# Kernel tuning notes

Measured on AMD Instinct MI355X. Metric: run time of the kernel, lower is better.

Reference implementation:

```python
import jax, jax.numpy as jnp
import numpy as np

EPS = 1e-5

def conv_act_norm(x, W, b, a, g, be):
    """1x1 Conv2d -> PReLU -> LayerNormalization4D (normalize over channel dim).
    x: [B,C,T,F]; W: [O,C]; b,g,be: [O]; a: PReLU scalar."""
    y = jnp.einsum('bctf,oc->botf', x, W) + b[None, :, None, None]
    y = jnp.where(y >= 0, y, a * y)
    mu = y.mean(axis=1, keepdims=True)
    var = y.var(axis=1, keepdims=True)
    y = (y - mu) * jax.lax.rsqrt(var + EPS)
    return y * g[None, :, None, None] + be[None, :, None, None]


def setup_inputs() -> dict:
    key = jax.random.key(0)
    B, C, T, F = 2, 64, 2048, 64
    H, HC = 4, 4            # n_head, hid_chan
    VC = C // H             # value channels per head = 16
    ks = jax.random.split(key, 16)
    s = 0.05
    inp = {
        'x': jax.random.normal(ks[0], (B, C, T, F), jnp.float32),
        # per-head Q projections (stacked along leading head axis)
        'Wq': jax.random.normal(ks[1], (H, HC, C), jnp.float32) * s,
        'bq': jnp.zeros((H, HC), jnp.float32),
        'aq': jnp.full((H,), 0.25, jnp.float32),
        'gq': jnp.ones((H, HC), jnp.float32),
        'betaq': jnp.zeros((H, HC), jnp.float32),
        # per-head K projections
        'Wk': jax.random.normal(ks[2], (H, HC, C), jnp.float32) * s,
        'bk': jnp.zeros((H, HC), jnp.float32),
        'ak': jnp.full((H,), 0.25, jnp.float32),
        'gk': jnp.ones((H, HC), jnp.float32),
        'betak': jnp.zeros((H, HC), jnp.float32),
        # per-head V projections
        'Wv': jax.random.normal(ks[3], (H, VC, C), jnp.float32) * s,
        'bv': jnp.zeros((H, VC), jnp.float32),
        'av': jnp.full((H,), 0.25, jnp.float32),
        'gv': jnp.ones((H, VC), jnp.float32),
        'betav': jnp.zeros((H, VC), jnp.float32),
        # output concat projection
        'Wp': jax.random.normal(ks[4], (C, C), jnp.float32) * s,
        'bp': jnp.zeros((C,), jnp.float32),
        'ap': jnp.asarray(0.25, jnp.float32),
        'gp': jnp.ones((C,), jnp.float32),
        'betap': jnp.zeros((C,), jnp.float32),
    }
    return inp


def reference(x, Wq, bq, aq, gq, betaq, Wk, bk, ak, gk, betak,
              Wv, bv, av, gv, betav, Wp, bp, ap, gp, betap):
    H = Wq.shape[0]
    B, C, T, F = x.shape
    per_head = jax.vmap(conv_act_norm, in_axes=(None, 0, 0, 0, 0, 0))
    Q = per_head(x, Wq, bq, aq, gq, betaq)      # [H,B,HC,T,F]
    K = per_head(x, Wk, bk, ak, gk, betak)      # [H,B,HC,T,F]
    V = per_head(x, Wv, bv, av, gv, betav)      # [H,B,VC,T,F]
    # flatten: sequence over time, embedding = channels*freq
    Qf = Q.transpose(0, 1, 3, 2, 4).reshape(H, B, T, -1)   # [H,B,T,HC*F]
    Kf = K.transpose(0, 1, 3, 2, 4).reshape(H, B, T, -1)
    Vt = V.transpose(0, 1, 3, 2, 4)                          # [H,B,T,VC,F]
    Vf = Vt.reshape(H, B, T, -1)                             # [H,B,T,VC*F]
    d = Qf.shape[-1]
    scale = jnp.asarray(1.0 / np.sqrt(d), x.dtype)
    attn = jnp.einsum('hbtd,hbsd->hbts', Qf, Kf) * scale    # [H,B,T,T]
    attn = jax.nn.softmax(attn, axis=-1)
    O = jnp.einsum('hbts,hbsd->hbtd', attn, Vf).reshape(Vt.shape)  # [H,B,T,VC,F]
    # back to [B, H*VC, T, F] with head-major channel ordering (matches torch view)
    O = O.transpose(1, 0, 3, 2, 4).reshape(B, C, T, F)
    out = conv_act_norm(O, Wp, bp, ap, gp, betap)
    return out + x
```

## Files before the change

kernel.cpp:

```cpp
#include <hip/hip_runtime.h>
#include <stdint.h>

typedef unsigned short ushort_t;
typedef unsigned int u32;
typedef short bf16x8 __attribute__((ext_vector_type(8)));
typedef float f32x4 __attribute__((ext_vector_type(4)));

#define MFMA16(a, b, c) __builtin_amdgcn_mfma_f32_16x16x32_bf16((a), (b), (c), 0, 0, 0)

__device__ __forceinline__ ushort_t f2bf(float f) {
  union { float f; u32 u; } v; v.f = f;
  return (ushort_t)((v.u + 0x7FFFu + ((v.u >> 16) & 1u)) >> 16);
}
__device__ __forceinline__ float bf2f(ushort_t h) {
  union { u32 u; float f; } v; v.u = ((u32)h) << 16;
  return v.f;
}

__device__ __forceinline__ void store_frag(ushort_t* __restrict__ arr, int hb, int t, int d, float v) {
  int lane = (t & 15) | (((d >> 3) & 3) << 4);
  size_t addr = ((((size_t)hb * 128 + (t >> 4)) * 8 + (d >> 5)) << 9) + ((size_t)lane << 3) + (d & 7);
  arr[addr] = f2bf(v);
}

__global__ __launch_bounds__(256) void k_proj_qkv(
    const float* __restrict__ x,
    const float* __restrict__ Wq, const float* __restrict__ bq, const float* __restrict__ aq,
    const float* __restrict__ gq, const float* __restrict__ beq,
    const float* __restrict__ Wk, const float* __restrict__ bk, const float* __restrict__ ak,
    const float* __restrict__ gk, const float* __restrict__ bek,
    const float* __restrict__ Wv, const float* __restrict__ bv, const float* __restrict__ av,
    const float* __restrict__ gv, const float* __restrict__ bev,
    ushort_t* __restrict__ Qp, ushort_t* __restrict__ Kp,
    ushort_t* __restrict__ Vp_hi, ushort_t* __restrict__ Vp_lo)
{
  int tid = blockIdx.x * 256 + threadIdx.x;
  int f = tid & 63;
  int t = (tid >> 6) & 2047;
  int b = tid >> 17;

  float qa[16], ka[16], va[64];
#pragma unroll
  for (int o = 0; o < 16; ++o) { qa[o] = bq[o]; ka[o] = bk[o]; }
#pragma unroll
  for (int o = 0; o < 64; ++o) va[o] = bv[o];

  const float* xp = x + ((size_t)b * 64 * 2048 + t) * 64 + f;
  for (int c = 0; c < 64; ++c) {
    float xv = xp[(size_t)c * (2048 * 64)];
#pragma unroll
    for (int o = 0; o < 16; ++o) qa[o] += Wq[o * 64 + c] * xv;
#pragma unroll
    for (int o = 0; o < 16; ++o) ka[o] += Wk[o * 64 + c] * xv;
#pragma unroll
    for (int o = 0; o < 64; ++o) va[o] += Wv[o * 64 + c] * xv;
  }

#pragma unroll
  for (int h = 0; h < 4; ++h) {
    int hb = h * 2 + b;
    {
      float aa = aq[h];
      float y[4]; float mu = 0.f;
#pragma unroll
      for (int j = 0; j < 4; ++j) { float u = qa[h * 4 + j]; u = u >= 0.f ? u : aa * u; y[j] = u; mu += u; }
      mu *= 0.25f;
      float var = 0.f;
#pragma unroll
      for (int j = 0; j < 4; ++j) { float d = y[j] - mu; var += d * d; }
      float is = rsqrtf(var * 0.25f + 1e-5f);
#pragma unroll
      for (int j = 0; j < 4; ++j) {
        float v = ((y[j] - mu) * is * gq[h * 4 + j] + beq[h * 4 + j]) * 0.0625f;
        store_frag(Qp, hb, t, j * 64 + f, v);
      }
    }
    {
      float aa = ak[h];
      float y[4]; float mu = 0.f;
#pragma unroll
      for (int j = 0; j < 4; ++j) { float u = ka[h * 4 + j]; u = u >= 0.f ? u : aa * u; y[j] = u; mu += u; }
      mu *= 0.25f;
      float var = 0.f;
#pragma unroll
      for (int j = 0; j < 4; ++j) { float d = y[j] - mu; var += d * d; }
      float is = rsqrtf(var * 0.25f + 1e-5f);
#pragma unroll
      for (int j = 0; j < 4; ++j) {
        float v = (y[j] - mu) * is * gk[h * 4 + j] + bek[h * 4 + j];
        store_frag(Kp, hb, t, j * 64 + f, v);
      }
    }
    {
      float aa = av[h];
      float y[16]; float mu = 0.f;
#pragma unroll
      for (int j = 0; j < 16; ++j) { float u = va[h * 16 + j]; u = u >= 0.f ? u : aa * u; y[j] = u; mu += u; }
      mu *= 0.0625f;
      float var = 0.f;
#pragma unroll
      for (int j = 0; j < 16; ++j) { float d = y[j] - mu; var += d * d; }
      float is = rsqrtf(var * 0.0625f + 1e-5f);
      int vlane = (f & 15) | (((t >> 3) & 3) << 4);
#pragma unroll
      for (int vc = 0; vc < 16; ++vc) {
        float v = (y[vc] - mu) * is * gv[h * 16 + vc] + bev[h * 16 + vc];
        int dvt = vc * 4 + (f >> 4);
        size_t addr = ((((size_t)hb * 64 + (t >> 5)) * 64 + dvt) << 9) + ((size_t)vlane << 3) + (t & 7);
        ushort_t hh = f2bf(v);
        Vp_hi[addr] = hh;
        Vp_lo[addr] = f2bf(v - bf2f(hh));
      }
    }
  }
}

__global__ __launch_bounds__(512, 4) void k_attn(
    const ushort_t* __restrict__ Qp, const ushort_t* __restrict__ Kp,
    const ushort_t* __restrict__ Vp_hi, const ushort_t* __restrict__ Vp_lo,
    float* __restrict__ O)
{
  extern __shared__ char smem[];
  ushort_t* Kbuf = (ushort_t*)smem;
  ushort_t* Qlds = (ushort_t*)(smem + 32768);
  ushort_t* Plds = (ushort_t*)(smem + 65536);
  float* pmax  = (float*)(smem + 69632);
  float* psum  = (float*)(smem + 70144);
  float* rsrow = (float*)(smem + 70656);
  float* lrow  = (float*)(smem + 70912);

  const int lane = threadIdx.x & 63;
  const int wid  = threadIdx.x >> 6;
  const int qblk = wid >> 1;
  const int tsh  = wid & 1;
  const int hb = blockIdx.x & 7;
  const int r2 = blockIdx.x >> 3;
  const int dvh = r2 & 1;
  const int qtile = r2 >> 1;
  const int tb4 = (lane >> 4) << 2;
  const int rowbase = qblk * 16 + tb4;

  {
    const ushort_t* qsrc = Qp + (((size_t)(hb * 128 + qtile * 4)) << 12) + ((size_t)lane << 3);
#pragma unroll
    for (int i = 0; i < 4; ++i) {
      int c = wid * 4 + i;
      uint4 v = *(const uint4*)(qsrc + ((size_t)c << 9));
      *(uint4*)(Qlds + ((size_t)c << 9) + ((size_t)lane << 3)) = v;
    }
    const ushort_t* ksrc = Kp + (((size_t)(hb * 128)) << 12) + ((size_t)lane << 3);
#pragma unroll
    for (int i = 0; i < 2; ++i) {
      int c = wid * 2 + i;
      uint4 v = *(const uint4*)(ksrc + ((size_t)c << 9));
      *(uint4*)(Kbuf + ((size_t)c << 9) + ((size_t)lane << 3)) = v;
    }
  }
  __syncthreads();

  f32x4 acc[16];
#pragma unroll
  for (int i = 0; i < 16; ++i) acc[i] = (f32x4){0.f, 0.f, 0.f, 0.f};
  float m_run[4], l_run[4];
#pragma unroll
  for (int r = 0; r < 4; ++r) { m_run[r] = -1e30f; l_run[r] = 0.f; }

  for (int s = 0; s < 64; ++s) {
    uint4 kst0, kst1;
    {
      int sn = (s + 1) & 63;
      const ushort_t* ksrc = Kp + (((size_t)(hb * 128 + 2 * sn)) << 12) + ((size_t)lane << 3);
      kst0 = *(const uint4*)(ksrc + ((size_t)(wid * 2 + 0) << 9));
      kst1 = *(const uint4*)(ksrc + ((size_t)(wid * 2 + 1) << 9));
    }

    const ushort_t* kb = Kbuf + (((size_t)(s & 1)) << 13);
    f32x4 sacc = (f32x4){0.f, 0.f, 0.f, 0.f};
    __builtin_amdgcn_s_setprio(1);
#pragma unroll
    for (int kk = 0; kk < 8; ++kk) {
      bf16x8 qf = *(const bf16x8*)(Qlds + (((size_t)(qblk * 8 + kk)) << 9) + ((size_t)lane << 3));
      bf16x8 kf = *(const bf16x8*)(kb + (((size_t)(tsh * 8 + kk)) << 9) + ((size_t)lane << 3));
      sacc = MFMA16(qf, kf, sacc);
    }
    __builtin_amdgcn_s_setprio(0);
    float rm[4];
#pragma unroll
    for (int r = 0; r < 4; ++r) rm[r] = sacc[r];
#pragma unroll
    for (int m = 1; m <= 8; m <<= 1) {
#pragma unroll
      for (int r = 0; r < 4; ++r) rm[r] = fmaxf(rm[r], __shfl_xor(rm[r], m));
    }
    if ((lane & 15) == 0)
      *(f32x4*)&pmax[tsh * 64 + rowbase] = (f32x4){rm[0], rm[1], rm[2], rm[3]};
    __syncthreads();

    f32x4 pm0 = *(const f32x4*)&pmax[rowbase];
    f32x4 pm1 = *(const f32x4*)&pmax[64 + rowbase];
    float rs[4], pv[4];
#pragma unroll
    for (int r = 0; r < 4; ++r) {
      float mn = fmaxf(m_run[r], fmaxf(pm0[r], pm1[r]));
      rs[r] = __expf(m_run[r] - mn);
      m_run[r] = mn;
      pv[r] = __expf(sacc[r] - mn);
    }
    float ps[4];
#pragma unroll
    for (int r = 0; r < 4; ++r) ps[r] = pv[r];
#pragma unroll
    for (int m = 1; m <= 8; m <<= 1) {
#pragma unroll
      for (int r = 0; r < 4; ++r) ps[r] += __shfl_xor(ps[r], m);
    }
    if ((lane & 15) == 0) {
      *(f32x4*)&psum[tsh * 64 + rowbase] = (f32x4){ps[0], ps[1], ps[2], ps[3]};
      if (tsh == 0)
        *(f32x4*)&rsrow[rowbase] = (f32x4){rs[0], rs[1], rs[2], rs[3]};
    }
    {
      int ts = tsh * 16 + (lane & 15);
      int cs = (ts >> 3) << 4;
      int jj = ts & 7;
#pragma unroll
      for (int r = 0; r < 4; ++r) {
        int tgt = (tb4 + r) | cs;
        Plds[(((size_t)qblk) << 9) + (tgt << 3) + jj] = f2bf(pv[r]);
      }
    }
    __syncthreads();

    {
      ushort_t* kdst = Kbuf + (((size_t)((s + 1) & 1)) << 13) + ((size_t)lane << 3);
      *(uint4*)(kdst + ((size_t)(wid * 2 + 0) << 9)) = kst0;
      *(uint4*)(kdst + ((size_t)(wid * 2 + 1) << 9)) = kst1;
    }

    {
      {
        f32x4 s0 = *(const f32x4*)&psum[rowbase];
        f32x4 s1 = *(const f32x4*)&psum[64 + rowbase];
#pragma unroll
        for (int r = 0; r < 4; ++r) l_run[r] = l_run[r] * rs[r] + s0[r] + s1[r];
      }
      const int dvt0 = dvh * 32 + wid * 4;
      const ushort_t* vh0 = Vp_hi + ((((size_t)hb * 64 + s) * 64 + dvt0) << 9) + ((size_t)lane << 3);
      const ushort_t* vl0 = Vp_lo + ((((size_t)hb * 64 + s) * 64 + dvt0) << 9) + ((size_t)lane << 3);
#pragma unroll
      for (int ip = 0; ip < 2; ++ip) {
        bf16x8 vh_a = *(const bf16x8*)(vh0 + ((size_t)(ip * 2 + 0) << 9));
        bf16x8 vl_a = *(const bf16x8*)(vl0 + ((size_t)(ip * 2 + 0) << 9));
        bf16x8 vh_b = *(const bf16x8*)(vh0 + ((size_t)(ip * 2 + 1) << 9));
        bf16x8 vl_b = *(const bf16x8*)(vl0 + ((size_t)(ip * 2 + 1) << 9));
        __builtin_amdgcn_s_setprio(1);
#pragma unroll
        for (int q = 0; q < 4; ++q) {
          bf16x8 pf = *(const bf16x8*)(Plds + (((size_t)q) << 9) + ((size_t)lane << 3));
          f32x4 rq = *(const f32x4*)&rsrow[q * 16 + tb4];
          int ia = q * 4 + ip * 2 + 0;
          int ib = q * 4 + ip * 2 + 1;
#pragma unroll
          for (int r = 0; r < 4; ++r) { acc[ia][r] *= rq[r]; acc[ib][r] *= rq[r]; }
          acc[ia] = MFMA16(pf, vh_a, acc[ia]);
          acc[ia] = MFMA16(pf, vl_a, acc[ia]);
          acc[ib] = MFMA16(pf, vh_b, acc[ib]);
          acc[ib] = MFMA16(pf, vl_b, acc[ib]);
        }
        __builtin_amdgcn_s_setprio(0);
      }
    }
    __syncthreads();
  }

  if (tsh == 0 && (lane & 15) == 0)
    *(f32x4*)&lrow[rowbase] = (f32x4){l_run[0], l_run[1], l_run[2], l_run[3]};
  __syncthreads();

  const int h = hb >> 1, b = hb & 1;
#pragma unroll
  for (int q = 0; q < 4; ++q) {
    f32x4 lq = *(const f32x4*)&lrow[q * 16 + tb4];
    f32x4 inv;
#pragma unroll
    for (int r = 0; r < 4; ++r) inv[r] = 1.0f / lq[r];
    int trow = qtile * 64 + q * 16 + tb4;
#pragma unroll
    for (int i = 0; i < 4; ++i) {
      int dv = dvh * 512 + wid * 64 + i * 16 + (lane & 15);
      float* op = O + (((size_t)b * 64 + h * 16 + (dv >> 6)) * 2048 + trow) * 64 + (dv & 63);
#pragma unroll
      for (int r = 0; r < 4; ++r) op[(size_t)r * 64] = acc[q * 4 + i][r] * inv[r];
    }
  }
}

__global__ __launch_bounds__(256) void k_outproj(
    const float* __restrict__ O, const float* __restrict__ Wp, const float* __restrict__ bp,
    const float* __restrict__ ap, const float* __restrict__ gp, const float* __restrict__ bep,
    const float* __restrict__ x, float* __restrict__ out)
{
  int tid = blockIdx.x * 256 + threadIdx.x;
  int f = tid & 63;
  int t = (tid >> 6) & 2047;
  int b = tid >> 17;

  float acc[64];
#pragma unroll
  for (int o = 0; o < 64; ++o) acc[o] = bp[o];
  const float* op_ = O + ((size_t)b * 64 * 2048 + t) * 64 + f;
  for (int c = 0; c < 64; ++c) {
    float ov = op_[(size_t)c * (2048 * 64)];
#pragma unroll
    for (int o = 0; o < 64; ++o) acc[o] += Wp[o * 64 + c] * ov;
  }
  float aa = ap[0];
  float mu = 0.f;
#pragma unroll
  for (int o = 0; o < 64; ++o) { float y = acc[o]; y = y >= 0.f ? y : aa * y; acc[o] = y; mu += y; }
  mu *= 0.015625f;
  float var = 0.f;
#pragma unroll
  for (int o = 0; o < 64; ++o) { float d = acc[o] - mu; var += d * d; }
  float is = rsqrtf(var * 0.015625f + 1e-5f);
  size_t base = ((size_t)b * 64 * 2048 + t) * 64 + f;
#pragma unroll
  for (int o = 0; o < 64; ++o) {
    size_t idx = base + (size_t)o * (2048 * 64);
    out[idx] = (acc[o] - mu) * is * gp[o] + bep[o] + x[idx];
  }
}

extern "C" void kernel_launch(void* const* d_in, const int* in_sizes, int n_in,
                              void* d_out, int out_size, void* d_ws, size_t ws_size,
                              hipStream_t stream) {
  (void)in_sizes; (void)n_in; (void)out_size; (void)ws_size;
  const float* x   = (const float*)d_in[0];
  const float* Wq  = (const float*)d_in[1];
  const float* bq  = (const float*)d_in[2];
  const float* aq  = (const float*)d_in[3];
  const float* gq  = (const float*)d_in[4];
  const float* beq = (const float*)d_in[5];
  const float* Wk  = (const float*)d_in[6];
  const float* bk  = (const float*)d_in[7];
  const float* ak  = (const float*)d_in[8];
  const float* gk  = (const float*)d_in[9];
  const float* bek = (const float*)d_in[10];
  const float* Wv  = (const float*)d_in[11];
  const float* bv  = (const float*)d_in[12];
  const float* av  = (const float*)d_in[13];
  const float* gv  = (const float*)d_in[14];
  const float* bev = (const float*)d_in[15];
  const float* Wp  = (const float*)d_in[16];
  const float* bp  = (const float*)d_in[17];
  const float* ap  = (const float*)d_in[18];
  const float* gp  = (const float*)d_in[19];
  const float* bep = (const float*)d_in[20];

  char* ws = (char*)d_ws;
  const size_t MB = 1024 * 1024;
  ushort_t* Qp    = (ushort_t*)(ws + 0 * MB);
  ushort_t* Kp    = (ushort_t*)(ws + 8 * MB);
  ushort_t* Vp_hi = (ushort_t*)(ws + 16 * MB);
  ushort_t* Vp_lo = (ushort_t*)(ws + 48 * MB);
  float*    Obuf  = (float*)(ws + 80 * MB);

  hipFuncSetAttribute((const void*)k_attn, hipFuncAttributeMaxDynamicSharedMemorySize, 71168);

  k_proj_qkv<<<1024, 256, 0, stream>>>(x, Wq, bq, aq, gq, beq, Wk, bk, ak, gk, bek,
                                       Wv, bv, av, gv, bev, Qp, Kp, Vp_hi, Vp_lo);
  k_attn<<<512, 512, 71168, stream>>>(Qp, Kp, Vp_hi, Vp_lo, Obuf);
  k_outproj<<<1024, 256, 0, stream>>>(Obuf, Wp, bp, ap, gp, bep, x, (float*)d_out);
}
```

Before: 555.6 us.

## Drop V lo-split, store O in bf16, stage QKV via LDS, lazy softmax rescale

V is no longer split into bf16 hi/lo halves, which halves the V MFMAs and V traffic in attention. The attention output is written as bf16 instead of fp32, shrinking the intermediate buffer that outproj reads. The QKV projection kernel now loads x into registers once, loops over heads, and stages results in LDS so global stores are coalesced 16-byte writes. The online softmax skips the accumulator rescale when the running max grows by at most 8, which avoids exp and multiply work but lets exponentials grow larger. The cost is lower precision in V and O.

```diff
diff --git a/kernel.cpp b/kernel.cpp
--- a/kernel.cpp
+++ b/kernel.cpp
@@ -17,13 +17,7 @@
   return v.f;
 }
 
-__device__ __forceinline__ void store_frag(ushort_t* __restrict__ arr, int hb, int t, int d, float v) {
-  int lane = (t & 15) | (((d >> 3) & 3) << 4);
-  size_t addr = ((((size_t)hb * 128 + (t >> 4)) * 8 + (d >> 5)) << 9) + ((size_t)lane << 3) + (d & 7);
-  arr[addr] = f2bf(v);
-}
-
-__global__ __launch_bounds__(256) void k_proj_qkv(
+__global__ __launch_bounds__(512, 4) void k_proj_qkv(
     const float* __restrict__ x,
     const float* __restrict__ Wq, const float* __restrict__ bq, const float* __restrict__ aq,
     const float* __restrict__ gq, const float* __restrict__ beq,
@@ -31,94 +25,122 @@
     const float* __restrict__ gk, const float* __restrict__ bek,
     const float* __restrict__ Wv, const float* __restrict__ bv, const float* __restrict__ av,
     const float* __restrict__ gv, const float* __restrict__ bev,
-    ushort_t* __restrict__ Qp, ushort_t* __restrict__ Kp,
-    ushort_t* __restrict__ Vp_hi, ushort_t* __restrict__ Vp_lo)
+    ushort_t* __restrict__ Qp, ushort_t* __restrict__ Kp, ushort_t* __restrict__ Vp)
 {
-  int tid = blockIdx.x * 256 + threadIdx.x;
-  int f = tid & 63;
-  int t = (tid >> 6) & 2047;
-  int b = tid >> 17;
-
-  float qa[16], ka[16], va[64];
-#pragma unroll
-  for (int o = 0; o < 16; ++o) { qa[o] = bq[o]; ka[o] = bk[o]; }
-#pragma unroll
-  for (int o = 0; o < 64; ++o) va[o] = bv[o];
-
-  const float* xp = x + ((size_t)b * 64 * 2048 + t) * 64 + f;
-  for (int c = 0; c < 64; ++c) {
-    float xv = xp[(size_t)c * (2048 * 64)];
-#pragma unroll
-    for (int o = 0; o < 16; ++o) qa[o] += Wq[o * 64 + c] * xv;
-#pragma unroll
-    for (int o = 0; o < 16; ++o) ka[o] += Wk[o * 64 + c] * xv;
-#pragma unroll
-    for (int o = 0; o < 64; ++o) va[o] += Wv[o * 64 + c] * xv;
-  }
-
-#pragma unroll
+  __shared__ ushort_t lds_q[16 * 136];
+  __shared__ ushort_t lds_k[16 * 136];
+  __shared__ ushort_t lds_v[512 * 24];
+
+  const int tid = threadIdx.x;
+  const int fi = tid & 31, ti = tid >> 5;
+  const int lane = tid & 63, wid = tid >> 6;
+  const int bid = blockIdx.x;
+  const int tt = bid & 127;
+  const int fh = (bid >> 7) & 1;
+  const int b  = bid >> 8;
+  const int t = tt * 16 + ti;
+  const int f = fh * 32 + fi;
+
+  float xr[64];
+  {
+    const float* xp = x + ((size_t)b * 64 * 2048 + t) * 64 + f;
+#pragma unroll
+    for (int c = 0; c < 64; ++c) xr[c] = xp[(size_t)c * (2048 * 64)];
+  }
+
+#pragma unroll 1
   for (int h = 0; h < 4; ++h) {
-    int hb = h * 2 + b;
-    {
-      float aa = aq[h];
-      float y[4]; float mu = 0.f;
-#pragma unroll
-      for (int j = 0; j < 4; ++j) { float u = qa[h * 4 + j]; u = u >= 0.f ? u : aa * u; y[j] = u; mu += u; }
+    const int hb = h * 2 + b;
+    float qa[4], ka[4], va[16];
+#pragma unroll
+    for (int j = 0; j < 4; ++j) { qa[j] = bq[h * 4 + j]; ka[j] = bk[h * 4 + j]; }
+#pragma unroll
+    for (int j = 0; j < 16; ++j) va[j] = bv[h * 16 + j];
+    for (int c = 0; c < 64; ++c) {
+      float xv = xr[c];
+#pragma unroll
+      for (int j = 0; j < 4; ++j) qa[j] += Wq[(h * 4 + j) * 64 + c] * xv;
+#pragma unroll
+      for (int j = 0; j < 4; ++j) ka[j] += Wk[(h * 4 + j) * 64 + c] * xv;
+#pragma unroll
+      for (int j = 0; j < 16; ++j) va[j] += Wv[(h * 16 + j) * 64 + c] * xv;
+    }
+    {
+      float aa = aq[h], mu = 0.f;
+#pragma unroll
+      for (int j = 0; j < 4; ++j) { float u = qa[j]; u = u >= 0.f ? u : aa * u; qa[j] = u; mu += u; }
       mu *= 0.25f;
       float var = 0.f;
 #pragma unroll
-      for (int j = 0; j < 4; ++j) { float d = y[j] - mu; var += d * d; }
+      for (int j = 0; j < 4; ++j) { float d = qa[j] - mu; var += d * d; }
       float is = rsqrtf(var * 0.25f + 1e-5f);
 #pragma unroll
       for (int j = 0; j < 4; ++j) {
-        float v = ((y[j] - mu) * is * gq[h * 4 + j] + beq[h * 4 + j]) * 0.0625f;
-        store_frag(Qp, hb, t, j * 64 + f, v);
-      }
-    }
-    {
-      float aa = ak[h];
-      float y[4]; float mu = 0.f;
-#pragma unroll
-      for (int j = 0; j < 4; ++j) { float u = ka[h * 4 + j]; u = u >= 0.f ? u : aa * u; y[j] = u; mu += u; }
+        float v = ((qa[j] - mu) * is * gq[h * 4 + j] + beq[h * 4 + j]) * 0.0625f;
+        lds_q[ti * 136 + j * 32 + fi] = f2bf(v);
+      }
+    }
+    {
+      float aa = ak[h], mu = 0.f;
+#pragma unroll
+      for (int j = 0; j < 4; ++j) { float u = ka[j]; u = u >= 0.f ? u : aa * u; ka[j] = u; mu += u; }
       mu *= 0.25f;
       float var = 0.f;
 #pragma unroll
-      for (int j = 0; j < 4; ++j) { float d = y[j] - mu; var += d * d; }
+      for (int j = 0; j < 4; ++j) { float d = ka[j] - mu; var += d * d; }
       float is = rsqrtf(var * 0.25f + 1e-5f);
 #pragma unroll
       for (int j = 0; j < 4; ++j) {
-        float v = (y[j] - mu) * is * gk[h * 4 + j] + bek[h * 4 + j];
-        store_frag(Kp, hb, t, j * 64 + f, v);
-      }
-    }
-    {
-      float aa = av[h];
-      float y[16]; float mu = 0.f;
-#pragma unroll
-      for (int j = 0; j < 16; ++j) { float u = va[h * 16 + j]; u = u >= 0.f ? u : aa * u; y[j] = u; mu += u; }
+        float v = (ka[j] - mu) * is * gk[h * 4 + j] + bek[h * 4 + j];
+        lds_k[ti * 136 + j * 32 + fi] = f2bf(v);
+      }
+    }
+    {
+      float aa = av[h], mu = 0.f;
+#pragma unroll
+      for (int j = 0; j < 16; ++j) { float u = va[j]; u = u >= 0.f ? u : aa * u; va[j] = u; mu += u; }
       mu *= 0.0625f;
       float var = 0.f;
 #pragma unroll
-      for (int j = 0; j < 16; ++j) { float d = y[j] - mu; var += d * d; }
+      for (int j = 0; j < 16; ++j) { float d = va[j] - mu; var += d * d; }
       float is = rsqrtf(var * 0.0625f + 1e-5f);
-      int vlane = (f & 15) | (((t >> 3) & 3) << 4);
 #pragma unroll
       for (int vc = 0; vc < 16; ++vc) {
-        float v = (y[vc] - mu) * is * gv[h * 16 + vc] + bev[h * 16 + vc];
-        int dvt = vc * 4 + (f >> 4);
-        size_t addr = ((((size_t)hb * 64 + (t >> 5)) * 64 + dvt) << 9) + ((size_t)vlane << 3) + (t & 7);
-        ushort_t hh = f2bf(v);
-        Vp_hi[addr] = hh;
-        Vp_lo[addr] = f2bf(v - bf2f(hh));
-      }
-    }
+        float v = (va[vc] - mu) * is * gv[h * 16 + vc] + bev[h * 16 + vc];
+        lds_v[(vc * 32 + fi) * 24 + ti] = f2bf(v);
+      }
+    }
+    __syncthreads();
+
+    {
+      int j = wid & 3;
+      const ushort_t* src = (wid < 4) ? lds_q : lds_k;
+      uint4 v = *(const uint4*)&src[(lane & 15) * 136 + j * 32 + ((lane >> 4) << 3)];
+      size_t base = ((((size_t)hb * 128 + tt) * 8) + (2 * j + fh)) << 9;
+      ushort_t* dst = (wid < 4) ? Qp : Kp;
+      *(uint4*)(dst + base + ((size_t)lane << 3)) = v;
+    }
+    {
+      const int halfsel = tt & 1;
+      const bool act = (lane >> 5) == halfsel;
+#pragma unroll
+      for (int i = 0; i < 4; ++i) {
+        int gl = wid * 4 + i;
+        int vc = gl >> 1, u = gl & 1;
+        int row = vc * 32 + u * 16 + (lane & 15);
+        uint4 v = *(const uint4*)&lds_v[row * 24 + (((lane >> 4) & 1) << 3)];
+        int g = vc * 4 + fh * 2 + u;
+        size_t base = (((size_t)hb * 64 + (tt >> 1)) * 64 + g) << 9;
+        if (act) *(uint4*)(Vp + base + ((size_t)lane << 3)) = v;
+      }
+    }
+    __syncthreads();
   }
 }
 
 __global__ __launch_bounds__(512, 4) void k_attn(
     const ushort_t* __restrict__ Qp, const ushort_t* __restrict__ Kp,
-    const ushort_t* __restrict__ Vp_hi, const ushort_t* __restrict__ Vp_lo,
-    float* __restrict__ O)
+    const ushort_t* __restrict__ Vp, ushort_t* __restrict__ O)
 {
   extern __shared__ char smem[];
   ushort_t* Kbuf = (ushort_t*)smem;
@@ -128,6 +150,7 @@
   float* psum  = (float*)(smem + 70144);
   float* rsrow = (float*)(smem + 70656);
   float* lrow  = (float*)(smem + 70912);
+  int*   skipf = (int*)(smem + 71168);
 
   const int lane = threadIdx.x & 63;
   const int wid  = threadIdx.x >> 6;
@@ -145,15 +168,13 @@
 #pragma unroll
     for (int i = 0; i < 4; ++i) {
       int c = wid * 4 + i;
-      uint4 v = *(const uint4*)(qsrc + ((size_t)c << 9));
-      *(uint4*)(Qlds + ((size_t)c << 9) + ((size_t)lane << 3)) = v;
+      *(uint4*)(Qlds + ((size_t)c << 9) + ((size_t)lane << 3)) = *(const uint4*)(qsrc + ((size_t)c << 9));
     }
     const ushort_t* ksrc = Kp + (((size_t)(hb * 128)) << 12) + ((size_t)lane << 3);
 #pragma unroll
     for (int i = 0; i < 2; ++i) {
       int c = wid * 2 + i;
-      uint4 v = *(const uint4*)(ksrc + ((size_t)c << 9));
-      *(uint4*)(Kbuf + ((size_t)c << 9) + ((size_t)lane << 3)) = v;
+      *(uint4*)(Kbuf + ((size_t)c << 9) + ((size_t)lane << 3)) = *(const uint4*)(ksrc + ((size_t)c << 9));
     }
   }
   __syncthreads();
@@ -198,14 +219,23 @@
 
     f32x4 pm0 = *(const f32x4*)&pmax[rowbase];
     f32x4 pm1 = *(const f32x4*)&pmax[64 + rowbase];
-    float rs[4], pv[4];
+    float mn[4], rs[4], pv[4];
+    int okl = 1;
 #pragma unroll
     for (int r = 0; r < 4; ++r) {
-      float mn = fmaxf(m_run[r], fmaxf(pm0[r], pm1[r]));
-      rs[r] = __expf(m_run[r] - mn);
-      m_run[r] = mn;
-      pv[r] = __expf(sacc[r] - mn);
-    }
+      mn[r] = fmaxf(m_run[r], fmaxf(pm0[r], pm1[r]));
+      okl &= (mn[r] - m_run[r] <= 8.0f) ? 1 : 0;
+    }
+    const int ok = __all(okl);
+    if (!ok) {
+#pragma unroll
+      for (int r = 0; r < 4; ++r) { rs[r] = __expf(m_run[r] - mn[r]); m_run[r] = mn[r]; }
+    } else {
+#pragma unroll
+      for (int r = 0; r < 4; ++r) rs[r] = 1.0f;
+    }
+#pragma unroll
+    for (int r = 0; r < 4; ++r) pv[r] = __expf(sacc[r] - m_run[r]);
     float ps[4];
 #pragma unroll
     for (int r = 0; r < 4; ++r) ps[r] = pv[r];
@@ -219,6 +249,7 @@
       if (tsh == 0)
         *(f32x4*)&rsrow[rowbase] = (f32x4){rs[0], rs[1], rs[2], rs[3]};
     }
+    if (tsh == 0 && lane == 0) skipf[qblk] = ok;
     {
       int ts = tsh * 16 + (lane & 15);
       int cs = (ts >> 3) << 4;
@@ -245,27 +276,24 @@
         for (int r = 0; r < 4; ++r) l_run[r] = l_run[r] * rs[r] + s0[r] + s1[r];
       }
       const int dvt0 = dvh * 32 + wid * 4;
-      const ushort_t* vh0 = Vp_hi + ((((size_t)hb * 64 + s) * 64 + dvt0) << 9) + ((size_t)lane << 3);
-      const ushort_t* vl0 = Vp_lo + ((((size_t)hb * 64 + s) * 64 + dvt0) << 9) + ((size_t)lane << 3);
+      const ushort_t* vh0 = Vp + ((((size_t)hb * 64 + s) * 64 + dvt0) << 9) + ((size_t)lane << 3);
 #pragma unroll
       for (int ip = 0; ip < 2; ++ip) {
         bf16x8 vh_a = *(const bf16x8*)(vh0 + ((size_t)(ip * 2 + 0) << 9));
-        bf16x8 vl_a = *(const bf16x8*)(vl0 + ((size_t)(ip * 2 + 0) << 9));
         bf16x8 vh_b = *(const bf16x8*)(vh0 + ((size_t)(ip * 2 + 1) << 9));
-        bf16x8 vl_b = *(const bf16x8*)(vl0 + ((size_t)(ip * 2 + 1) << 9));
         __builtin_amdgcn_s_setprio(1);
 #pragma unroll
         for (int q = 0; q < 4; ++q) {
           bf16x8 pf = *(const bf16x8*)(Plds + (((size_t)q) << 9) + ((size_t)lane << 3));
-          f32x4 rq = *(const f32x4*)&rsrow[q * 16 + tb4];
           int ia = q * 4 + ip * 2 + 0;
           int ib = q * 4 + ip * 2 + 1;
-#pragma unroll
-          for (int r = 0; r < 4; ++r) { acc[ia][r] *= rq[r]; acc[ib][r] *= rq[r]; }
+          if (!skipf[q]) {
+            f32x4 rq = *(const f32x4*)&rsrow[q * 16 + tb4];
+#pragma unroll
+            for (int r = 0; r < 4; ++r) { acc[ia][r] *= rq[r]; acc[ib][r] *= rq[r]; }
+          }
           acc[ia] = MFMA16(pf, vh_a, acc[ia]);
-          acc[ia] = MFMA16(pf, vl_a, acc[ia]);
           acc[ib] = MFMA16(pf, vh_b, acc[ib]);
-          acc[ib] = MFMA16(pf, vl_b, acc[ib]);
         }
         __builtin_amdgcn_s_setprio(0);
       }
@@ -288,15 +316,15 @@
 #pragma unroll
     for (int i = 0; i < 4; ++i) {
       int dv = dvh * 512 + wid * 64 + i * 16 + (lane & 15);
-      float* op = O + (((size_t)b * 64 + h * 16 + (dv >> 6)) * 2048 + trow) * 64 + (dv & 63);
-#pragma unroll
-      for (int r = 0; r < 4; ++r) op[(size_t)r * 64] = acc[q * 4 + i][r] * inv[r];
+      ushort_t* op = O + (((size_t)b * 64 + h * 16 + (dv >> 6)) * 2048 + trow) * 64 + (dv & 63);
+#pragma unroll
+      for (int r = 0; r < 4; ++r) op[(size_t)r * 64] = f2bf(acc[q * 4 + i][r] * inv[r]);
     }
   }
 }
 
 __global__ __launch_bounds__(256) void k_outproj(
-    const float* __restrict__ O, const float* __restrict__ Wp, const float* __restrict__ bp,
+    const ushort_t* __restrict__ O, const float* __restrict__ Wp, const float* __restrict__ bp,
     const float* __restrict__ ap, const float* __restrict__ gp, const float* __restrict__ bep,
     const float* __restrict__ x, float* __restrict__ out)
 {
@@ -308,9 +336,9 @@
   float acc[64];
 #pragma unroll
   for (int o = 0; o < 64; ++o) acc[o] = bp[o];
-  const float* op_ = O + ((size_t)b * 64 * 2048 + t) * 64 + f;
+  const ushort_t* op_ = O + ((size_t)b * 64 * 2048 + t) * 64 + f;
   for (int c = 0; c < 64; ++c) {
-    float ov = op_[(size_t)c * (2048 * 64)];
+    float ov = bf2f(op_[(size_t)c * (2048 * 64)]);
 #pragma unroll
     for (int o = 0; o < 64; ++o) acc[o] += Wp[o * 64 + c] * ov;
   }
@@ -359,16 +387,15 @@
 
   char* ws = (char*)d_ws;
   const size_t MB = 1024 * 1024;
-  ushort_t* Qp    = (ushort_t*)(ws + 0 * MB);
-  ushort_t* Kp    = (ushort_t*)(ws + 8 * MB);
-  ushort_t* Vp_hi = (ushort_t*)(ws + 16 * MB);
-  ushort_t* Vp_lo = (ushort_t*)(ws + 48 * MB);
-  float*    Obuf  = (float*)(ws + 80 * MB);
-
-  hipFuncSetAttribute((const void*)k_attn, hipFuncAttributeMaxDynamicSharedMemorySize, 71168);
-
-  k_proj_qkv<<<1024, 256, 0, stream>>>(x, Wq, bq, aq, gq, beq, Wk, bk, ak, gk, bek,
-                                       Wv, bv, av, gv, bev, Qp, Kp, Vp_hi, Vp_lo);
-  k_attn<<<512, 512, 71168, stream>>>(Qp, Kp, Vp_hi, Vp_lo, Obuf);
+  ushort_t* Qp   = (ushort_t*)(ws + 0 * MB);
+  ushort_t* Kp   = (ushort_t*)(ws + 8 * MB);
+  ushort_t* Vp   = (ushort_t*)(ws + 16 * MB);
+  ushort_t* Obuf = (ushort_t*)(ws + 48 * MB);
+
+  hipFuncSetAttribute((const void*)k_attn, hipFuncAttributeMaxDynamicSharedMemorySize, 71296);
+
+  k_proj_qkv<<<512, 512, 0, stream>>>(x, Wq, bq, aq, gq, beq, Wk, bk, ak, gk, bek,
+                                      Wv, bv, av, gv, bev, Qp, Kp, Vp);
+  k_attn<<<512, 512, 71296, stream>>>(Qp, Kp, Vp, Obuf);
   k_outproj<<<1024, 256, 0, stream>>>(Obuf, Wp, bp, ap, gp, bep, x, (float*)d_out);
 }
```

After: 520.2 us. -6.4%, faster.
